# Optimization experiments

Hardware: AMD Instinct MI355X
Metric: run time of the kernel (lower is better)

## Reference

```python
import jax, jax.numpy as jnp
import numpy as np

NSAMPLE = 64
RADIUS = 0.08
EPS = 1e-5
B, N, M, C = 4, 16384, 1024, 256


def ball_query(xyz, new_xyz, radius, nsample):
    """xyz [B,N,3], new_xyz [B,M,3] -> idx [B,M,nsample] int32.
    Picks first `nsample` points within `radius` of each query (in point order),
    padding with the first found index (0 if none), matching pointnet2 CUDA op."""
    b, n = xyz.shape[0], xyz.shape[1]
    m = new_xyz.shape[1]
    # squared distances via norms + matmul (avoids [B,M,N,3] intermediate)
    d2 = (jnp.sum(new_xyz * new_xyz, -1)[:, :, None]
          + jnp.sum(xyz * xyz, -1)[:, None, :]
          - 2.0 * jnp.einsum('bmc,bnc->bmn', new_xyz, xyz))  # [B,M,N]
    mask = d2 < radius * radius
    rank = jnp.cumsum(mask.astype(jnp.int32), axis=-1) - 1   # slot of each valid point
    valid = mask & (rank < nsample)
    slots = jnp.where(valid, rank, nsample)                  # invalid -> dump slot
    n_idx = jnp.broadcast_to(jnp.arange(n, dtype=jnp.int32), (b, m, n))
    b_idx = jnp.arange(b)[:, None, None]
    m_idx = jnp.arange(m)[None, :, None]
    idx = jnp.zeros((b, m, nsample + 1), jnp.int32)
    idx = idx.at[b_idx, m_idx, slots].set(n_idx)[..., :nsample]
    cnt = jnp.sum(mask, axis=-1)                             # [B,M] neighbors found
    pad = jnp.arange(nsample)[None, None, :] >= cnt[:, :, None]
    idx = jnp.where(pad, idx[:, :, :1], idx)                 # pad with first index
    return idx


def _mlp_layer(x, W, bias, gamma, beta, mu, var):
    # 1x1 conv (pointwise) + BatchNorm (eval, running stats) + ReLU, channels-last
    y = jnp.einsum('bmsc,oc->bmso', x, W) + bias
    y = (y - mu) * (gamma * jax.lax.rsqrt(var + EPS)) + beta
    return jax.nn.relu(y)


def reference(seed_xyz_fps, seed_xyz_graspable, seed_features_graspable,
              W1, b1, g1, be1, m1, v1, W2, b2, g2, be2, m2, v2):
    idx = ball_query(seed_xyz_fps, seed_xyz_graspable, RADIUS, NSAMPLE)  # [B,M,S]
    # gather + relative coordinates (use_xyz=True, normalize_xyz=False)
    gxyz = jax.vmap(lambda p, i: p[i])(seed_xyz_fps, idx)                # [B,M,S,3]
    gxyz = gxyz - seed_xyz_graspable[:, :, None, :]
    feats = jnp.swapaxes(seed_features_graspable, 1, 2)                  # [B,N,C]
    gfeat = jax.vmap(lambda f, i: f[i])(feats, idx)                      # [B,M,S,C]
    x = jnp.concatenate([gxyz, gfeat], axis=-1)                          # [B,M,S,3+C]
    x = _mlp_layer(x, W1, b1, g1, be1, m1, v1)                           # [B,M,S,256]
    x = _mlp_layer(x, W2, b2, g2, be2, m2, v2)                           # [B,M,S,256]
    x = jnp.max(x, axis=2)                                               # [B,M,256]
    return jnp.swapaxes(x, 1, 2)                                         # [B,256,M]


def setup_inputs() -> dict:
    key = jax.random.key(0)
    ks = jax.random.split(key, 16)
    return {
        'seed_xyz_fps': jax.random.uniform(ks[0], (B, N, 3), jnp.float32),
        'seed_xyz_graspable': jax.random.uniform(ks[1], (B, M, 3), jnp.float32),
        'seed_features_graspable': jax.random.normal(ks[2], (B, C, N), jnp.float32),
        'W1': jax.random.normal(ks[3], (256, 3 + C), jnp.float32) * 0.05,
        'b1': jax.random.normal(ks[4], (256,), jnp.float32) * 0.05,
        'g1': jax.random.uniform(ks[5], (256,), jnp.float32, 0.5, 1.5),
        'be1': jax.random.normal(ks[6], (256,), jnp.float32) * 0.05,
        'm1': jax.random.normal(ks[7], (256,), jnp.float32) * 0.1,
        'v1': jax.random.uniform(ks[8], (256,), jnp.float32, 0.5, 1.5),
        'W2': jax.random.normal(ks[9], (256, 256), jnp.float32) * 0.05,
        'b2': jax.random.normal(ks[10], (256,), jnp.float32) * 0.05,
        'g2': jax.random.uniform(ks[11], (256,), jnp.float32, 0.5, 1.5),
        'be2': jax.random.normal(ks[12], (256,), jnp.float32) * 0.05,
        'm2': jax.random.normal(ks[13], (256,), jnp.float32) * 0.1,
        'v2': jax.random.uniform(ks[14], (256,), jnp.float32, 0.5, 1.5),
    }
```

## Files before the change

kernel.cpp:

```cpp
#include <hip/hip_runtime.h>
#include <stdint.h>

typedef __bf16 bf16x8 __attribute__((ext_vector_type(8)));
typedef float f32x4 __attribute__((ext_vector_type(4)));

#define NSAMPLE 64
static constexpr int Bb = 4, Nn = 16384, Mm = 1024, Cc = 256;
static constexpr int K1P = 288;

__device__ __forceinline__ unsigned short f2bf(float f) {
  unsigned int u = __builtin_bit_cast(unsigned int, f);
  u = u + 0x7fffu + ((u >> 16) & 1u);
  return (unsigned short)(u >> 16);
}

__device__ __forceinline__ void gload_lds16(const void* g, void* lds) {
  __builtin_amdgcn_global_load_lds(
      (const __attribute__((address_space(1))) uint32_t*)g,
      (__attribute__((address_space(3))) uint32_t*)lds, 16, 0, 0);
}

__global__ void helpers_kernel(const float* __restrict__ xyz,
                               const float* __restrict__ new_xyz,
                               const float* __restrict__ feats,
                               const float* __restrict__ W1, const float* __restrict__ b1,
                               const float* __restrict__ g1, const float* __restrict__ be1,
                               const float* __restrict__ m1, const float* __restrict__ v1,
                               const float* __restrict__ W2, const float* __restrict__ b2,
                               const float* __restrict__ g2, const float* __restrict__ be2,
                               const float* __restrict__ m2, const float* __restrict__ v2,
                               unsigned short* __restrict__ W1b, float* __restrict__ b1e,
                               unsigned short* __restrict__ W2b, float* __restrict__ b2e,
                               unsigned short* __restrict__ featsT,
                               int* __restrict__ idx) {
  __shared__ float tile[64][65];
  __shared__ int wl[4][4][64];
  __shared__ int wcnt[4][4];
  int bx = blockIdx.x;
  int t = threadIdx.x;
  if (bx < 1024) {
    const float r2 = (float)(0.08 * 0.08);
    int bm0 = bx * 4;
    int lane = t & 63, w = t >> 6;
    int b = bm0 >> 10;
    float qx[4], qy[4], qz[4], qq[4];
    int cnt[4];
#pragma unroll
    for (int qi = 0; qi < 4; qi++) {
      qx[qi] = new_xyz[(bm0 + qi) * 3];
      qy[qi] = new_xyz[(bm0 + qi) * 3 + 1];
      qz[qi] = new_xyz[(bm0 + qi) * 3 + 2];
      qq[qi] = __fadd_rn(__fadd_rn(__fmul_rn(qx[qi], qx[qi]), __fmul_rn(qy[qi], qy[qi])),
                         __fmul_rn(qz[qi], qz[qi]));
      cnt[qi] = 0;
    }
    const float* P = xyz + ((size_t)b * Nn + w * 4096) * 3;
    for (int n0 = 0; n0 < 4096; n0 += 64) {
      const float* pp = P + (n0 + lane) * 3;
      float x = pp[0], y = pp[1], z = pp[2];
      float p2 = __fadd_rn(__fadd_rn(__fmul_rn(x, x), __fmul_rn(y, y)), __fmul_rn(z, z));
#pragma unroll
      for (int qi = 0; qi < 4; qi++) {
        if (cnt[qi] >= NSAMPLE) continue;
        float dt = __fadd_rn(__fadd_rn(__fmul_rn(qx[qi], x), __fmul_rn(qy[qi], y)),
                             __fmul_rn(qz[qi], z));
        float d2 = __fsub_rn(__fadd_rn(qq[qi], p2), __fmul_rn(2.f, dt));
        bool valid = d2 < r2;
        unsigned long long mask = __ballot(valid);
        if (mask) {
          if (valid) {
            int pos = cnt[qi] + __popcll(mask & ((1ull << lane) - 1ull));
            if (pos < NSAMPLE) wl[qi][w][pos] = w * 4096 + n0 + lane;
          }
          cnt[qi] += (int)__popcll(mask);
        }
      }
      if (cnt[0] >= NSAMPLE && cnt[1] >= NSAMPLE && cnt[2] >= NSAMPLE && cnt[3] >= NSAMPLE)
        break;
    }
    if (lane == 0) {
#pragma unroll
      for (int qi = 0; qi < 4; qi++) wcnt[qi][w] = cnt[qi];
    }
    __syncthreads();
    {
      int qi = t >> 6, s = t & 63;
      int c0 = wcnt[qi][0], c1 = wcnt[qi][1], c2 = wcnt[qi][2], c3 = wcnt[qi][3];
      int tot = c0 + c1 + c2 + c3;
      int cc = tot < NSAMPLE ? tot : NSAMPLE;
      int v;
      if (s < cc) {
        if (s < c0) v = wl[qi][0][s];
        else if (s < c0 + c1) v = wl[qi][1][s - c0];
        else if (s < c0 + c1 + c2) v = wl[qi][2][s - c0 - c1];
        else v = wl[qi][3][s - c0 - c1 - c2];
      } else {
        v = (c0 > 0) ? wl[qi][0][0] : (c1 > 0) ? wl[qi][1][0]
          : (c2 > 0) ? wl[qi][2][0] : (c3 > 0) ? wl[qi][3][0] : 0;
      }
      idx[(size_t)(bm0 + qi) * NSAMPLE + s] = v;
    }
    return;
  }
  if (bx < 5120) {
    int fb = bx - 1024;
    int b = fb >> 10;
    int rem = fb & 1023;
    int nt = rem >> 2, ct = rem & 3;
    int tx = t & 63, ty = t >> 6;
    const float* src = feats + ((size_t)b * Cc + ct * 64) * Nn + nt * 64;
#pragma unroll
    for (int i = 0; i < 16; i++) {
      int c = i * 4 + ty;
      tile[c][tx] = src[(size_t)c * Nn + tx];
    }
    __syncthreads();
    unsigned short* dst = featsT + ((size_t)b * Nn + nt * 64) * Cc + ct * 64;
    int c4 = (t & 15) * 4, n0 = t >> 4;
#pragma unroll
    for (int i = 0; i < 4; i++) {
      int n = i * 16 + n0;
      ushort4 v;
      v.x = f2bf(tile[c4][n]);
      v.y = f2bf(tile[c4 + 1][n]);
      v.z = f2bf(tile[c4 + 2][n]);
      v.w = f2bf(tile[c4 + 3][n]);
      *(ushort4*)&dst[(size_t)n * Cc + c4] = v;
    }
    return;
  }
  int g = (bx - 5120) * 256 + t;
  if (g < 256 * K1P) {
    int o = g / K1P, k = g - o * K1P;
    float s = g1[o] / sqrtf(v1[o] + 1e-5f);
    float w = 0.f;
    if (k < 256) w = W1[o * 259 + 3 + k];
    else if (k < 259) w = W1[o * 259 + (k - 256)];
    W1b[g] = f2bf(w * s);
  }
  if (g < 256 * 256) {
    int o = g >> 8;
    float s = g2[o] / sqrtf(v2[o] + 1e-5f);
    W2b[g] = f2bf(W2[g] * s);
  }
  if (g < 256) {
    float s1 = g1[g] / sqrtf(v1[g] + 1e-5f);
    b1e[g] = s1 * (b1[g] - m1[g]) + be1[g];
    float s2 = g2[g] / sqrtf(v2[g] + 1e-5f);
    b2e[g] = s2 * (b2[g] - m2[g]) + be2[g];
  }
}

__global__ __launch_bounds__(256, 4) void fused_kernel(
    const unsigned short* __restrict__ featsT, const float* __restrict__ xyz,
    const float* __restrict__ new_xyz, const int* __restrict__ idx,
    const unsigned short* __restrict__ W1b, const float* __restrict__ b1e,
    const unsigned short* __restrict__ W2b, const float* __restrict__ b2e,
    float* __restrict__ out) {
  __shared__ unsigned short Xf[64 * 256];
  __shared__ unsigned short Xco[64 * 40];
  int t = threadIdx.x;
  int wave = t >> 6, lane = t & 63;
  int lr = lane & 15, kg = lane >> 4;
  int wcol = wave * 64;
  int bm = blockIdx.x;
  int b = bm >> 10;

  {
    int idxr = idx[(size_t)bm * NSAMPLE + wave * 16 + (lane & 15)];
#pragma unroll
    for (int i = 0; i < 8; i++) {
      int j = wave * 8 + i;
      int iv = __shfl(idxr, 2 * i + (lane >> 5));
      int r7 = (2 * j + (lane >> 5)) & 7;
      int cg = (lane & 31) ^ r7;
      gload_lds16(featsT + ((size_t)b * Nn + iv) * Cc + cg * 8, &Xf[j * 512]);
    }
  }
  if (t < 64) {
    int ci = idx[(size_t)bm * NSAMPLE + t];
    const float* pp = xyz + ((size_t)b * Nn + ci) * 3;
    float px = pp[0], py = pp[1], pz = pp[2];
    unsigned int c01 = (unsigned int)f2bf(px - new_xyz[bm * 3])
                     | ((unsigned int)f2bf(py - new_xyz[bm * 3 + 1]) << 16);
    unsigned int c2 = (unsigned int)f2bf(pz - new_xyz[bm * 3 + 2]);
    uint4 v0 = make_uint4(c01, c2, 0u, 0u);
    uint4 z = make_uint4(0u, 0u, 0u, 0u);
    uint4* row = (uint4*)&Xco[t * 40];
    row[0] = v0; row[1] = z; row[2] = z; row[3] = z; row[4] = z;
  }
  __syncthreads();

  f32x4 acc[4][4];
#pragma unroll
  for (int mi = 0; mi < 4; mi++)
#pragma unroll
    for (int ni = 0; ni < 4; ni++) acc[mi][ni] = (f32x4){0.f, 0.f, 0.f, 0.f};
  {
    bf16x8 w[2][4];
#pragma unroll
    for (int ni = 0; ni < 4; ni++)
      w[0][ni] = *(const bf16x8*)&W1b[(size_t)(wcol + ni * 16 + lr) * K1P + kg * 8];
#pragma unroll
    for (int kk = 0; kk < 9; kk++) {
      int cur = kk & 1, nxt = cur ^ 1;
      if (kk < 8) {
#pragma unroll
        for (int ni = 0; ni < 4; ni++)
          w[nxt][ni] =
              *(const bf16x8*)&W1b[(size_t)(wcol + ni * 16 + lr) * K1P + (kk + 1) * 32 + kg * 8];
      }
      bf16x8 a[4];
#pragma unroll
      for (int mi = 0; mi < 4; mi++) {
        int r = mi * 16 + lr;
        if (kk < 8) {
          int cs = ((kk * 4 + kg) ^ (r & 7)) * 8;
          a[mi] = *(const bf16x8*)&Xf[r * 256 + cs];
        } else {
          a[mi] = *(const bf16x8*)&Xco[r * 40 + kg * 8];
        }
      }
#pragma unroll
      for (int mi = 0; mi < 4; mi++)
#pragma unroll
        for (int ni = 0; ni < 4; ni++)
          acc[mi][ni] =
              __builtin_amdgcn_mfma_f32_16x16x32_bf16(a[mi], w[cur][ni], acc[mi][ni], 0, 0, 0);
    }
  }
  __syncthreads();

#pragma unroll
  for (int ni = 0; ni < 4; ni++) {
    int o = wcol + ni * 16 + lr;
    float bb = b1e[o];
#pragma unroll
    for (int mi = 0; mi < 4; mi++)
#pragma unroll
      for (int j = 0; j < 4; j++) {
        int r = mi * 16 + kg * 4 + j;
        float h = fmaxf(acc[mi][ni][j] + bb, 0.f);
        Xf[r * 256 + ((((o >> 3) ^ (r & 7)) << 3) + (o & 7))] = f2bf(h);
      }
  }
  __syncthreads();

#pragma unroll
  for (int mi = 0; mi < 4; mi++)
#pragma unroll
    for (int ni = 0; ni < 4; ni++) acc[mi][ni] = (f32x4){0.f, 0.f, 0.f, 0.f};
  {
    bf16x8 w[2][4];
#pragma unroll
    for (int ni = 0; ni < 4; ni++)
      w[0][ni] = *(const bf16x8*)&W2b[(size_t)(wcol + ni * 16 + lr) * 256 + kg * 8];
#pragma unroll
    for (int kk = 0; kk < 8; kk++) {
      int cur = kk & 1, nxt = cur ^ 1;
      if (kk < 7) {
#pragma unroll
        for (int ni = 0; ni < 4; ni++)
          w[nxt][ni] =
              *(const bf16x8*)&W2b[(size_t)(wcol + ni * 16 + lr) * 256 + (kk + 1) * 32 + kg * 8];
      }
      bf16x8 a[4];
#pragma unroll
      for (int mi = 0; mi < 4; mi++) {
        int r = mi * 16 + lr;
        int cs = ((kk * 4 + kg) ^ (r & 7)) * 8;
        a[mi] = *(const bf16x8*)&Xf[r * 256 + cs];
      }
#pragma unroll
      for (int mi = 0; mi < 4; mi++)
#pragma unroll
        for (int ni = 0; ni < 4; ni++)
          acc[mi][ni] =
              __builtin_amdgcn_mfma_f32_16x16x32_bf16(a[mi], w[cur][ni], acc[mi][ni], 0, 0, 0);
    }
  }
  {
    int m = bm & (Mm - 1);
#pragma unroll
    for (int ni = 0; ni < 4; ni++) {
      float bv = b2e[wcol + ni * 16 + lr];
      float v = 0.f;
#pragma unroll
      for (int mi = 0; mi < 4; mi++)
#pragma unroll
        for (int j = 0; j < 4; j++) v = fmaxf(v, acc[mi][ni][j] + bv);
      v = fmaxf(v, __shfl_xor(v, 16));
      v = fmaxf(v, __shfl_xor(v, 32));
      if (kg == 0)
        out[((size_t)b * 256 + wcol + ni * 16 + lr) * Mm + m] = v;
    }
  }
}

extern "C" void kernel_launch(void* const* d_in, const int* in_sizes, int n_in,
                              void* d_out, int out_size, void* d_ws, size_t ws_size,
                              hipStream_t stream) {
  (void)in_sizes; (void)n_in; (void)out_size; (void)ws_size;
  const float* xyz     = (const float*)d_in[0];
  const float* new_xyz = (const float*)d_in[1];
  const float* feats   = (const float*)d_in[2];
  const float* W1 = (const float*)d_in[3];
  const float* b1 = (const float*)d_in[4];
  const float* g1 = (const float*)d_in[5];
  const float* be1 = (const float*)d_in[6];
  const float* m1 = (const float*)d_in[7];
  const float* v1 = (const float*)d_in[8];
  const float* W2 = (const float*)d_in[9];
  const float* b2 = (const float*)d_in[10];
  const float* g2 = (const float*)d_in[11];
  const float* be2 = (const float*)d_in[12];
  const float* m2 = (const float*)d_in[13];
  const float* v2 = (const float*)d_in[14];
  float* out = (float*)d_out;

  char* ws = (char*)d_ws;
  unsigned short* W1b   = (unsigned short*)(ws + 0);
  unsigned short* W2b   = (unsigned short*)(ws + 147456);
  float*          b1e   = (float*)(ws + 278528);
  float*          b2e   = (float*)(ws + 279552);
  unsigned short* featsT= (unsigned short*)(ws + 280576);
  int*            idx   = (int*)(ws + 33835008);

  helpers_kernel<<<1024 + 4096 + 288, 256, 0, stream>>>(
      xyz, new_xyz, feats, W1, b1, g1, be1, m1, v1, W2, b2, g2, be2, m2, v2,
      W1b, b1e, W2b, b2e, featsT, idx);
  fused_kernel<<<Bb * Mm, 256, 0, stream>>>(featsT, xyz, new_xyz, idx,
                                            W1b, b1e, W2b, b2e, out);
}
```

Measured before the change: 152.7 us.

## Split output columns across 8 waves per block and drop weight double-buffering

The fused MLP kernel now runs 512 threads (8 waves) per block, each wave owning 32 output channels instead of 64. The gather of feature rows into shared memory is spread across the 8 waves as well. The register double-buffering of weight fragments is removed in favour of a simple per-k load. The aim is more waves per CU and lower register pressure to hide gather and load latency, at the cost of less per-wave reuse of the A fragments and unhidden weight load latency.

```diff
diff --git a/kernel.cpp b/kernel.cpp
--- a/kernel.cpp
+++ b/kernel.cpp
@@ -151,7 +151,7 @@
   }
 }
 
-__global__ __launch_bounds__(256, 4) void fused_kernel(
+__global__ __launch_bounds__(512, 6) void fused_kernel(
     const unsigned short* __restrict__ featsT, const float* __restrict__ xyz,
     const float* __restrict__ new_xyz, const int* __restrict__ idx,
     const unsigned short* __restrict__ W1b, const float* __restrict__ b1e,
@@ -162,15 +162,15 @@
   int t = threadIdx.x;
   int wave = t >> 6, lane = t & 63;
   int lr = lane & 15, kg = lane >> 4;
-  int wcol = wave * 64;
+  int wcol = wave * 32;
   int bm = blockIdx.x;
   int b = bm >> 10;
 
   {
-    int idxr = idx[(size_t)bm * NSAMPLE + wave * 16 + (lane & 15)];
-#pragma unroll
-    for (int i = 0; i < 8; i++) {
-      int j = wave * 8 + i;
+    int idxr = idx[(size_t)bm * NSAMPLE + wave * 8 + (lane & 7)];
+#pragma unroll
+    for (int i = 0; i < 4; i++) {
+      int j = wave * 4 + i;
       int iv = __shfl(idxr, 2 * i + (lane >> 5));
       int r7 = (2 * j + (lane >> 5)) & 7;
       int cg = (lane & 31) ^ r7;
@@ -191,48 +191,38 @@
   }
   __syncthreads();
 
-  f32x4 acc[4][4];
+  f32x4 acc[4][2];
 #pragma unroll
   for (int mi = 0; mi < 4; mi++)
 #pragma unroll
-    for (int ni = 0; ni < 4; ni++) acc[mi][ni] = (f32x4){0.f, 0.f, 0.f, 0.f};
-  {
-    bf16x8 w[2][4];
-#pragma unroll
-    for (int ni = 0; ni < 4; ni++)
-      w[0][ni] = *(const bf16x8*)&W1b[(size_t)(wcol + ni * 16 + lr) * K1P + kg * 8];
-#pragma unroll
-    for (int kk = 0; kk < 9; kk++) {
-      int cur = kk & 1, nxt = cur ^ 1;
+    for (int ni = 0; ni < 2; ni++) acc[mi][ni] = (f32x4){0.f, 0.f, 0.f, 0.f};
+#pragma unroll
+  for (int kk = 0; kk < 9; kk++) {
+    bf16x8 w[2];
+#pragma unroll
+    for (int ni = 0; ni < 2; ni++)
+      w[ni] = *(const bf16x8*)&W1b[(size_t)(wcol + ni * 16 + lr) * K1P + kk * 32 + kg * 8];
+    bf16x8 a[4];
+#pragma unroll
+    for (int mi = 0; mi < 4; mi++) {
+      int r = mi * 16 + lr;
       if (kk < 8) {
-#pragma unroll
-        for (int ni = 0; ni < 4; ni++)
-          w[nxt][ni] =
-              *(const bf16x8*)&W1b[(size_t)(wcol + ni * 16 + lr) * K1P + (kk + 1) * 32 + kg * 8];
+        int cs = ((kk * 4 + kg) ^ (r & 7)) * 8;
+        a[mi] = *(const bf16x8*)&Xf[r * 256 + cs];
+      } else {
+        a[mi] = *(const bf16x8*)&Xco[r * 40 + kg * 8];
       }
-      bf16x8 a[4];
-#pragma unroll
-      for (int mi = 0; mi < 4; mi++) {
-        int r = mi * 16 + lr;
-        if (kk < 8) {
-          int cs = ((kk * 4 + kg) ^ (r & 7)) * 8;
-          a[mi] = *(const bf16x8*)&Xf[r * 256 + cs];
-        } else {
-          a[mi] = *(const bf16x8*)&Xco[r * 40 + kg * 8];
-        }
-      }
-#pragma unroll
-      for (int mi = 0; mi < 4; mi++)
-#pragma unroll
-        for (int ni = 0; ni < 4; ni++)
-          acc[mi][ni] =
-              __builtin_amdgcn_mfma_f32_16x16x32_bf16(a[mi], w[cur][ni], acc[mi][ni], 0, 0, 0);
-    }
+    }
+#pragma unroll
+    for (int mi = 0; mi < 4; mi++)
+#pragma unroll
+      for (int ni = 0; ni < 2; ni++)
+        acc[mi][ni] = __builtin_amdgcn_mfma_f32_16x16x32_bf16(a[mi], w[ni], acc[mi][ni], 0, 0, 0);
   }
   __syncthreads();
 
 #pragma unroll
-  for (int ni = 0; ni < 4; ni++) {
+  for (int ni = 0; ni < 2; ni++) {
     int o = wcol + ni * 16 + lr;
     float bb = b1e[o];
 #pragma unroll
@@ -249,40 +239,30 @@
 #pragma unroll
   for (int mi = 0; mi < 4; mi++)
 #pragma unroll
-    for (int ni = 0; ni < 4; ni++) acc[mi][ni] = (f32x4){0.f, 0.f, 0.f, 0.f};
-  {
-    bf16x8 w[2][4];
-#pragma unroll
-    for (int ni = 0; ni < 4; ni++)
-      w[0][ni] = *(const bf16x8*)&W2b[(size_t)(wcol + ni * 16 + lr) * 256 + kg * 8];
-#pragma unroll
-    for (int kk = 0; kk < 8; kk++) {
-      int cur = kk & 1, nxt = cur ^ 1;
-      if (kk < 7) {
-#pragma unroll
-        for (int ni = 0; ni < 4; ni++)
-          w[nxt][ni] =
-              *(const bf16x8*)&W2b[(size_t)(wcol + ni * 16 + lr) * 256 + (kk + 1) * 32 + kg * 8];
-      }
-      bf16x8 a[4];
-#pragma unroll
-      for (int mi = 0; mi < 4; mi++) {
-        int r = mi * 16 + lr;
-        int cs = ((kk * 4 + kg) ^ (r & 7)) * 8;
-        a[mi] = *(const bf16x8*)&Xf[r * 256 + cs];
-      }
-#pragma unroll
-      for (int mi = 0; mi < 4; mi++)
-#pragma unroll
-        for (int ni = 0; ni < 4; ni++)
-          acc[mi][ni] =
-              __builtin_amdgcn_mfma_f32_16x16x32_bf16(a[mi], w[cur][ni], acc[mi][ni], 0, 0, 0);
-    }
+    for (int ni = 0; ni < 2; ni++) acc[mi][ni] = (f32x4){0.f, 0.f, 0.f, 0.f};
+#pragma unroll
+  for (int kk = 0; kk < 8; kk++) {
+    bf16x8 w[2];
+#pragma unroll
+    for (int ni = 0; ni < 2; ni++)
+      w[ni] = *(const bf16x8*)&W2b[(size_t)(wcol + ni * 16 + lr) * 256 + kk * 32 + kg * 8];
+    bf16x8 a[4];
+#pragma unroll
+    for (int mi = 0; mi < 4; mi++) {
+      int r = mi * 16 + lr;
+      int cs = ((kk * 4 + kg) ^ (r & 7)) * 8;
+      a[mi] = *(const bf16x8*)&Xf[r * 256 + cs];
+    }
+#pragma unroll
+    for (int mi = 0; mi < 4; mi++)
+#pragma unroll
+      for (int ni = 0; ni < 2; ni++)
+        acc[mi][ni] = __builtin_amdgcn_mfma_f32_16x16x32_bf16(a[mi], w[ni], acc[mi][ni], 0, 0, 0);
   }
   {
     int m = bm & (Mm - 1);
 #pragma unroll
-    for (int ni = 0; ni < 4; ni++) {
+    for (int ni = 0; ni < 2; ni++) {
       float bv = b2e[wcol + ni * 16 + lr];
       float v = 0.f;
 #pragma unroll
@@ -329,6 +309,6 @@
   helpers_kernel<<<1024 + 4096 + 288, 256, 0, stream>>>(
       xyz, new_xyz, feats, W1, b1, g1, be1, m1, v1, W2, b2, g2, be2, m2, v2,
       W1b, b1e, W2b, b2e, featsT, idx);
-  fused_kernel<<<Bb * Mm, 256, 0, stream>>>(featsT, xyz, new_xyz, idx,
+  fused_kernel<<<Bb * Mm, 512, 0, stream>>>(featsT, xyz, new_xyz, idx,
                                             W1b, b1e, W2b, b2e, out);
 }
```

Result: slower. 158.2 us (+3.6%).

## Precompute layer-1 feature projection per point before gathering neighbors

Applied to the files above, without the earlier changes.

Layer 1 is linear in the gathered features, so the 256x256 feature part of W1 is applied once per source point (B*N=65536 rows) instead of once per gathered neighbor (B*M*64=262144 rows). The result is stored as bf16 X1all and gathered in place of the transposed features. The xyz term, bias and ReLU are then added per neighbor in fp32 on the vector units. A separate prep kernel folds the weights and biases. This cuts layer-1 matmul work by about 4x, but adds an extra bf16 rounding of the pre-activation and one more kernel launch, and the removed double-buffered weight prefetch may expose load latency.

```diff
diff --git a/kernel.cpp b/kernel.cpp
--- a/kernel.cpp
+++ b/kernel.cpp
@@ -6,13 +6,15 @@
 
 #define NSAMPLE 64
 static constexpr int Bb = 4, Nn = 16384, Mm = 1024, Cc = 256;
-static constexpr int K1P = 288;
 
 __device__ __forceinline__ unsigned short f2bf(float f) {
   unsigned int u = __builtin_bit_cast(unsigned int, f);
   u = u + 0x7fffu + ((u >> 16) & 1u);
   return (unsigned short)(u >> 16);
 }
+__device__ __forceinline__ float bf2f(unsigned short u) {
+  return __builtin_bit_cast(float, (unsigned int)u << 16);
+}
 
 __device__ __forceinline__ void gload_lds16(const void* g, void* lds) {
   __builtin_amdgcn_global_load_lds(
@@ -20,25 +22,46 @@
       (__attribute__((address_space(3))) uint32_t*)lds, 16, 0, 0);
 }
 
-__global__ void helpers_kernel(const float* __restrict__ xyz,
-                               const float* __restrict__ new_xyz,
-                               const float* __restrict__ feats,
-                               const float* __restrict__ W1, const float* __restrict__ b1,
-                               const float* __restrict__ g1, const float* __restrict__ be1,
-                               const float* __restrict__ m1, const float* __restrict__ v1,
-                               const float* __restrict__ W2, const float* __restrict__ b2,
-                               const float* __restrict__ g2, const float* __restrict__ be2,
-                               const float* __restrict__ m2, const float* __restrict__ v2,
-                               unsigned short* __restrict__ W1b, float* __restrict__ b1e,
-                               unsigned short* __restrict__ W2b, float* __restrict__ b2e,
-                               unsigned short* __restrict__ featsT,
-                               int* __restrict__ idx) {
-  __shared__ float tile[64][65];
-  __shared__ int wl[4][4][64];
-  __shared__ int wcnt[4][4];
+__global__ void prep_kernel(const float* __restrict__ W1, const float* __restrict__ b1,
+                            const float* __restrict__ g1, const float* __restrict__ be1,
+                            const float* __restrict__ m1, const float* __restrict__ v1,
+                            const float* __restrict__ W2, const float* __restrict__ b2,
+                            const float* __restrict__ g2, const float* __restrict__ be2,
+                            const float* __restrict__ m2, const float* __restrict__ v2,
+                            unsigned short* __restrict__ W1b, float* __restrict__ w1c,
+                            float* __restrict__ b1e,
+                            unsigned short* __restrict__ W2b, float* __restrict__ b2e) {
+  int t = blockIdx.x * 256 + threadIdx.x;
+  {
+    int o = t >> 8, k = t & 255;
+    float s1 = g1[o] / sqrtf(v1[o] + 1e-5f);
+    W1b[t] = f2bf(W1[o * 259 + 3 + k] * s1);
+    float s2 = g2[o] / sqrtf(v2[o] + 1e-5f);
+    W2b[t] = f2bf(W2[t] * s2);
+  }
+  if (t < 256 * 3) {
+    int o = t / 3, c = t - o * 3;
+    float s = g1[o] / sqrtf(v1[o] + 1e-5f);
+    w1c[t] = W1[o * 259 + c] * s;
+  }
+  if (t < 256) {
+    float s1 = g1[t] / sqrtf(v1[t] + 1e-5f);
+    b1e[t] = s1 * (b1[t] - m1[t]) + be1[t];
+    float s2 = g2[t] / sqrtf(v2[t] + 1e-5f);
+    b2e[t] = s2 * (b2[t] - m2[t]) + be2[t];
+  }
+}
+
+__global__ __launch_bounds__(256) void ballq_x1all_kernel(
+    const float* __restrict__ xyz, const float* __restrict__ new_xyz,
+    const float* __restrict__ feats, const unsigned short* __restrict__ W1b,
+    unsigned short* __restrict__ X1all, int* __restrict__ idx) {
+  __shared__ __align__(16) char smem[16640 + 32768];
   int bx = blockIdx.x;
   int t = threadIdx.x;
   if (bx < 1024) {
+    int* wl = (int*)smem;
+    int* wcnt = (int*)(smem + 4096);
     const float r2 = (float)(0.08 * 0.08);
     int bm0 = bx * 4;
     int lane = t & 63, w = t >> 6;
@@ -70,7 +93,7 @@
         if (mask) {
           if (valid) {
             int pos = cnt[qi] + __popcll(mask & ((1ull << lane) - 1ull));
-            if (pos < NSAMPLE) wl[qi][w][pos] = w * 4096 + n0 + lane;
+            if (pos < NSAMPLE) wl[(qi * 4 + w) * 64 + pos] = w * 4096 + n0 + lane;
           }
           cnt[qi] += (int)__popcll(mask);
         }
@@ -80,85 +103,114 @@
     }
     if (lane == 0) {
 #pragma unroll
-      for (int qi = 0; qi < 4; qi++) wcnt[qi][w] = cnt[qi];
+      for (int qi = 0; qi < 4; qi++) wcnt[qi * 4 + w] = cnt[qi];
     }
     __syncthreads();
     {
       int qi = t >> 6, s = t & 63;
-      int c0 = wcnt[qi][0], c1 = wcnt[qi][1], c2 = wcnt[qi][2], c3 = wcnt[qi][3];
+      int c0 = wcnt[qi * 4], c1 = wcnt[qi * 4 + 1], c2 = wcnt[qi * 4 + 2], c3 = wcnt[qi * 4 + 3];
       int tot = c0 + c1 + c2 + c3;
       int cc = tot < NSAMPLE ? tot : NSAMPLE;
       int v;
       if (s < cc) {
-        if (s < c0) v = wl[qi][0][s];
-        else if (s < c0 + c1) v = wl[qi][1][s - c0];
-        else if (s < c0 + c1 + c2) v = wl[qi][2][s - c0 - c1];
-        else v = wl[qi][3][s - c0 - c1 - c2];
+        if (s < c0) v = wl[(qi * 4 + 0) * 64 + s];
+        else if (s < c0 + c1) v = wl[(qi * 4 + 1) * 64 + s - c0];
+        else if (s < c0 + c1 + c2) v = wl[(qi * 4 + 2) * 64 + s - c0 - c1];
+        else v = wl[(qi * 4 + 3) * 64 + s - c0 - c1 - c2];
       } else {
-        v = (c0 > 0) ? wl[qi][0][0] : (c1 > 0) ? wl[qi][1][0]
-          : (c2 > 0) ? wl[qi][2][0] : (c3 > 0) ? wl[qi][3][0] : 0;
+        v = (c0 > 0) ? wl[(qi * 4 + 0) * 64] : (c1 > 0) ? wl[(qi * 4 + 1) * 64]
+          : (c2 > 0) ? wl[(qi * 4 + 2) * 64] : (c3 > 0) ? wl[(qi * 4 + 3) * 64] : 0;
       }
       idx[(size_t)(bm0 + qi) * NSAMPLE + s] = v;
     }
     return;
   }
-  if (bx < 5120) {
-    int fb = bx - 1024;
-    int b = fb >> 10;
-    int rem = fb & 1023;
-    int nt = rem >> 2, ct = rem & 3;
+  float(*ftile)[65] = (float(*)[65])smem;
+  unsigned short* Xf = (unsigned short*)(smem + 16640);
+  int xb = bx - 1024;
+  int b = xb >> 8, nt = xb & 255, n0 = nt * 64;
+  for (int ct = 0; ct < 4; ct++) {
+    const float* src = feats + ((size_t)(b * Cc + ct * 64)) * Nn + n0;
     int tx = t & 63, ty = t >> 6;
-    const float* src = feats + ((size_t)b * Cc + ct * 64) * Nn + nt * 64;
 #pragma unroll
     for (int i = 0; i < 16; i++) {
       int c = i * 4 + ty;
-      tile[c][tx] = src[(size_t)c * Nn + tx];
+      ftile[c][tx] = src[(size_t)c * Nn + tx];
     }
     __syncthreads();
-    unsigned short* dst = featsT + ((size_t)b * Nn + nt * 64) * Cc + ct * 64;
-    int c4 = (t & 15) * 4, n0 = t >> 4;
+    int c4 = (t & 15) * 4, nr = t >> 4;
 #pragma unroll
     for (int i = 0; i < 4; i++) {
-      int n = i * 16 + n0;
+      int n = i * 16 + nr;
+      int cg = ct * 8 + (c4 >> 3);
+      int sc = cg ^ (n & 7);
       ushort4 v;
-      v.x = f2bf(tile[c4][n]);
-      v.y = f2bf(tile[c4 + 1][n]);
-      v.z = f2bf(tile[c4 + 2][n]);
-      v.w = f2bf(tile[c4 + 3][n]);
-      *(ushort4*)&dst[(size_t)n * Cc + c4] = v;
-    }
-    return;
-  }
-  int g = (bx - 5120) * 256 + t;
-  if (g < 256 * K1P) {
-    int o = g / K1P, k = g - o * K1P;
-    float s = g1[o] / sqrtf(v1[o] + 1e-5f);
-    float w = 0.f;
-    if (k < 256) w = W1[o * 259 + 3 + k];
-    else if (k < 259) w = W1[o * 259 + (k - 256)];
-    W1b[g] = f2bf(w * s);
-  }
-  if (g < 256 * 256) {
-    int o = g >> 8;
-    float s = g2[o] / sqrtf(v2[o] + 1e-5f);
-    W2b[g] = f2bf(W2[g] * s);
-  }
-  if (g < 256) {
-    float s1 = g1[g] / sqrtf(v1[g] + 1e-5f);
-    b1e[g] = s1 * (b1[g] - m1[g]) + be1[g];
-    float s2 = g2[g] / sqrtf(v2[g] + 1e-5f);
-    b2e[g] = s2 * (b2[g] - m2[g]) + be2[g];
+      v.x = f2bf(ftile[c4][n]);
+      v.y = f2bf(ftile[c4 + 1][n]);
+      v.z = f2bf(ftile[c4 + 2][n]);
+      v.w = f2bf(ftile[c4 + 3][n]);
+      *(ushort4*)&Xf[n * 256 + sc * 8 + (c4 & 7)] = v;
+    }
+    __syncthreads();
+  }
+  int wave = t >> 6, lane = t & 63;
+  int lr = lane & 15, kg = lane >> 4;
+  int wcol = wave * 64;
+  f32x4 acc[4][4];
+#pragma unroll
+  for (int mi = 0; mi < 4; mi++)
+#pragma unroll
+    for (int ni = 0; ni < 4; ni++) acc[mi][ni] = (f32x4){0.f, 0.f, 0.f, 0.f};
+#pragma unroll
+  for (int kk = 0; kk < 8; kk++) {
+    bf16x8 w[4];
+#pragma unroll
+    for (int ni = 0; ni < 4; ni++)
+      w[ni] = *(const bf16x8*)&W1b[(size_t)(wcol + ni * 16 + lr) * 256 + kk * 32 + kg * 8];
+    bf16x8 a[4];
+#pragma unroll
+    for (int mi = 0; mi < 4; mi++) {
+      int r = mi * 16 + lr;
+      int cs = ((kk * 4 + kg) ^ (r & 7)) * 8;
+      a[mi] = *(const bf16x8*)&Xf[r * 256 + cs];
+    }
+#pragma unroll
+    for (int mi = 0; mi < 4; mi++)
+#pragma unroll
+      for (int ni = 0; ni < 4; ni++)
+        acc[mi][ni] = __builtin_amdgcn_mfma_f32_16x16x32_bf16(a[mi], w[ni], acc[mi][ni], 0, 0, 0);
+  }
+  __syncthreads();
+#pragma unroll
+  for (int ni = 0; ni < 4; ni++) {
+    int o = wcol + ni * 16 + lr;
+#pragma unroll
+    for (int mi = 0; mi < 4; mi++)
+#pragma unroll
+      for (int j = 0; j < 4; j++) {
+        int r = mi * 16 + kg * 4 + j;
+        Xf[r * 256 + o] = f2bf(acc[mi][ni][j]);
+      }
+  }
+  __syncthreads();
+  {
+    int row = t >> 2, off = (t & 3) * 64;
+    unsigned short* dst = X1all + ((size_t)(b * Nn + n0 + row)) * 256 + off;
+#pragma unroll
+    for (int i = 0; i < 8; i++)
+      *(uint4*)(dst + i * 8) = *(const uint4*)&Xf[row * 256 + off + i * 8];
   }
 }
 
 __global__ __launch_bounds__(256, 4) void fused_kernel(
-    const unsigned short* __restrict__ featsT, const float* __restrict__ xyz,
+    const unsigned short* __restrict__ X1all, const float* __restrict__ xyz,
     const float* __restrict__ new_xyz, const int* __restrict__ idx,
-    const unsigned short* __restrict__ W1b, const float* __restrict__ b1e,
+    const float* __restrict__ w1c, const float* __restrict__ b1e,
     const unsigned short* __restrict__ W2b, const float* __restrict__ b2e,
     float* __restrict__ out) {
   __shared__ unsigned short Xf[64 * 256];
-  __shared__ unsigned short Xco[64 * 40];
+  __shared__ float Xc[3][64];
+  __shared__ float Cw[4][256];
   int t = threadIdx.x;
   int wave = t >> 6, lane = t & 63;
   int lr = lane & 15, kg = lane >> 4;
@@ -174,110 +226,68 @@
       int iv = __shfl(idxr, 2 * i + (lane >> 5));
       int r7 = (2 * j + (lane >> 5)) & 7;
       int cg = (lane & 31) ^ r7;
-      gload_lds16(featsT + ((size_t)b * Nn + iv) * Cc + cg * 8, &Xf[j * 512]);
+      gload_lds16(X1all + ((size_t)b * Nn + iv) * Cc + cg * 8, &Xf[j * 512]);
     }
   }
   if (t < 64) {
     int ci = idx[(size_t)bm * NSAMPLE + t];
     const float* pp = xyz + ((size_t)b * Nn + ci) * 3;
-    float px = pp[0], py = pp[1], pz = pp[2];
-    unsigned int c01 = (unsigned int)f2bf(px - new_xyz[bm * 3])
-                     | ((unsigned int)f2bf(py - new_xyz[bm * 3 + 1]) << 16);
-    unsigned int c2 = (unsigned int)f2bf(pz - new_xyz[bm * 3 + 2]);
-    uint4 v0 = make_uint4(c01, c2, 0u, 0u);
-    uint4 z = make_uint4(0u, 0u, 0u, 0u);
-    uint4* row = (uint4*)&Xco[t * 40];
-    row[0] = v0; row[1] = z; row[2] = z; row[3] = z; row[4] = z;
+    Xc[0][t] = pp[0] - new_xyz[bm * 3];
+    Xc[1][t] = pp[1] - new_xyz[bm * 3 + 1];
+    Xc[2][t] = pp[2] - new_xyz[bm * 3 + 2];
+  }
+  {
+    Cw[0][t] = b1e[t];
+    Cw[1][t] = w1c[t * 3];
+    Cw[2][t] = w1c[t * 3 + 1];
+    Cw[3][t] = w1c[t * 3 + 2];
   }
   __syncthreads();
 
+  {
+    int s = t >> 2, c0 = (t & 3) * 64;
+    float cx = Xc[0][s], cy = Xc[1][s], cz = Xc[2][s];
+#pragma unroll
+    for (int g = 0; g < 8; g++) {
+      int cg = (c0 >> 3) + g;
+      int sc = cg ^ (s & 7);
+      unsigned short* p = &Xf[s * 256 + sc * 8];
+      uint4 v = *(uint4*)p;
+      unsigned short* e = (unsigned short*)&v;
+#pragma unroll
+      for (int j = 0; j < 8; j++) {
+        int o = cg * 8 + j;
+        float h = bf2f(e[j]) + Cw[0][o] + cx * Cw[1][o] + cy * Cw[2][o] + cz * Cw[3][o];
+        e[j] = f2bf(fmaxf(h, 0.f));
+      }
+      *(uint4*)p = v;
+    }
+  }
+  __syncthreads();
+
   f32x4 acc[4][4];
 #pragma unroll
   for (int mi = 0; mi < 4; mi++)
 #pragma unroll
     for (int ni = 0; ni < 4; ni++) acc[mi][ni] = (f32x4){0.f, 0.f, 0.f, 0.f};
-  {
-    bf16x8 w[2][4];
+#pragma unroll
+  for (int kk = 0; kk < 8; kk++) {
+    bf16x8 w[4];
 #pragma unroll
     for (int ni = 0; ni < 4; ni++)
-      w[0][ni] = *(const bf16x8*)&W1b[(size_t)(wcol + ni * 16 + lr) * K1P + kg * 8];
-#pragma unroll
-    for (int kk = 0; kk < 9; kk++) {
-      int cur = kk & 1, nxt = cur ^ 1;
-      if (kk < 8) {
-#pragma unroll
-        for (int ni = 0; ni < 4; ni++)
-          w[nxt][ni] =
-              *(const bf16x8*)&W1b[(size_t)(wcol + ni * 16 + lr) * K1P + (kk + 1) * 32 + kg * 8];
-      }
-      bf16x8 a[4];
-#pragma unroll
-      for (int mi = 0; mi < 4; mi++) {
-        int r = mi * 16 + lr;
-        if (kk < 8) {
-          int cs = ((kk * 4 + kg) ^ (r & 7)) * 8;
-          a[mi] = *(const bf16x8*)&Xf[r * 256 + cs];
-        } else {
-          a[mi] = *(const bf16x8*)&Xco[r * 40 + kg * 8];
-        }
-      }
-#pragma unroll
-      for (int mi = 0; mi < 4; mi++)
-#pragma unroll
-        for (int ni = 0; ni < 4; ni++)
-          acc[mi][ni] =
-              __builtin_amdgcn_mfma_f32_16x16x32_bf16(a[mi], w[cur][ni], acc[mi][ni], 0, 0, 0);
-    }
-  }
-  __syncthreads();
-
-#pragma unroll
-  for (int ni = 0; ni < 4; ni++) {
-    int o = wcol + ni * 16 + lr;
-    float bb = b1e[o];
+      w[ni] = *(const bf16x8*)&W2b[(size_t)(wcol + ni * 16 + lr) * 256 + kk * 32 + kg * 8];
+    bf16x8 a[4];
+#pragma unroll
+    for (int mi = 0; mi < 4; mi++) {
+      int r = mi * 16 + lr;
+      int cs = ((kk * 4 + kg) ^ (r & 7)) * 8;
+      a[mi] = *(const bf16x8*)&Xf[r * 256 + cs];
+    }
 #pragma unroll
     for (int mi = 0; mi < 4; mi++)
 #pragma unroll
-      for (int j = 0; j < 4; j++) {
-        int r = mi * 16 + kg * 4 + j;
-        float h = fmaxf(acc[mi][ni][j] + bb, 0.f);
-        Xf[r * 256 + ((((o >> 3) ^ (r & 7)) << 3) + (o & 7))] = f2bf(h);
-      }
-  }
-  __syncthreads();
-
-#pragma unroll
-  for (int mi = 0; mi < 4; mi++)
-#pragma unroll
-    for (int ni = 0; ni < 4; ni++) acc[mi][ni] = (f32x4){0.f, 0.f, 0.f, 0.f};
-  {
-    bf16x8 w[2][4];
-#pragma unroll
-    for (int ni = 0; ni < 4; ni++)
-      w[0][ni] = *(const bf16x8*)&W2b[(size_t)(wcol + ni * 16 + lr) * 256 + kg * 8];
-#pragma unroll
-    for (int kk = 0; kk < 8; kk++) {
-      int cur = kk & 1, nxt = cur ^ 1;
-      if (kk < 7) {
-#pragma unroll
-        for (int ni = 0; ni < 4; ni++)
-          w[nxt][ni] =
-              *(const bf16x8*)&W2b[(size_t)(wcol + ni * 16 + lr) * 256 + (kk + 1) * 32 + kg * 8];
-      }
-      bf16x8 a[4];
-#pragma unroll
-      for (int mi = 0; mi < 4; mi++) {
-        int r = mi * 16 + lr;
-        int cs = ((kk * 4 + kg) ^ (r & 7)) * 8;
-        a[mi] = *(const bf16x8*)&Xf[r * 256 + cs];
-      }
-#pragma unroll
-      for (int mi = 0; mi < 4; mi++)
-#pragma unroll
-        for (int ni = 0; ni < 4; ni++)
-          acc[mi][ni] =
-              __builtin_amdgcn_mfma_f32_16x16x32_bf16(a[mi], w[cur][ni], acc[mi][ni], 0, 0, 0);
-    }
+      for (int ni = 0; ni < 4; ni++)
+        acc[mi][ni] = __builtin_amdgcn_mfma_f32_16x16x32_bf16(a[mi], w[ni], acc[mi][ni], 0, 0, 0);
   }
   {
     int m = bm & (Mm - 1);
@@ -320,15 +330,16 @@
 
   char* ws = (char*)d_ws;
   unsigned short* W1b   = (unsigned short*)(ws + 0);
-  unsigned short* W2b   = (unsigned short*)(ws + 147456);
-  float*          b1e   = (float*)(ws + 278528);
-  float*          b2e   = (float*)(ws + 279552);
-  unsigned short* featsT= (unsigned short*)(ws + 280576);
-  int*            idx   = (int*)(ws + 33835008);
-
-  helpers_kernel<<<1024 + 4096 + 288, 256, 0, stream>>>(
-      xyz, new_xyz, feats, W1, b1, g1, be1, m1, v1, W2, b2, g2, be2, m2, v2,
-      W1b, b1e, W2b, b2e, featsT, idx);
-  fused_kernel<<<Bb * Mm, 256, 0, stream>>>(featsT, xyz, new_xyz, idx,
-                                            W1b, b1e, W2b, b2e, out);
-}
+  unsigned short* W2b   = (unsigned short*)(ws + 131072);
+  float*          w1c   = (float*)(ws + 262144);
+  float*          b1e   = (float*)(ws + 265216);
+  float*          b2e   = (float*)(ws + 266240);
+  unsigned short* X1all = (unsigned short*)(ws + 267264);
+  int*            idx   = (int*)(ws + 33821696);
+
+  prep_kernel<<<256, 256, 0, stream>>>(
+      W1, b1, g1, be1, m1, v1, W2, b2, g2, be2, m2, v2, W1b, w1c, b1e, W2b, b2e);
+  ballq_x1all_kernel<<<1024 + 1024, 256, 0, stream>>>(xyz, new_xyz, feats, W1b, X1all, idx);
+  fused_kernel<<<Bb * Mm, 256, 0, stream>>>(X1all, xyz, new_xyz, idx,
+                                            w1c, b1e, W2b, b2e, out);
+}
```

Result: slower. 169.3 us (+10.8%).
